# Kernel optimization log

Measured on AMD Instinct MI355X. Metric: run time of the kernel, lower is better.

The kernel has to match this reference:

```python
import jax, jax.numpy as jnp
import numpy as np

EPS = 1e-07
NUM_ELEMENTS = 33554432  # cooptimizer.rest_mesh_blob.num_elements
GRID = (256, 256, 256)   # voxel design grid


def setup_inputs() -> dict:
    key = jax.random.key(0)
    k1, k2 = jax.random.split(key)
    voxel = jax.random.uniform(k1, GRID, dtype=jnp.float32)
    # voxel -> element id map (the keys of blob_to_fish_cell / cell_indices)
    cell_indices = jax.random.randint(k2, GRID, 0, NUM_ELEMENTS, dtype=jnp.int64 if jax.config.jax_enable_x64 else jnp.int32)
    return {"voxel": voxel, "cell_indices": cell_indices, "num_elements": NUM_ELEMENTS}


def reference(voxel, cell_indices, num_elements):
    # clamp matches voxel.clamp(0, 1) (output is value-independent, but kept for fidelity)
    _ = jnp.clip(voxel, 0.0, 1.0)
    # vectorized replacement of `for k in keys: elements[k] = 1.0`
    elements = jnp.zeros((num_elements,), dtype=voxel.dtype).at[cell_indices.reshape(-1)].set(1.0)
    return elements + EPS
```

## Files before the change

kernel.cpp:

```cpp
#include <hip/hip_runtime.h>
#include <hip/hip_bf16.h>

#define EPS   1e-07f
#define ONEPS (1.0f + 1e-07f)

typedef int          iv4 __attribute__((ext_vector_type(4)));
typedef float        fv4 __attribute__((ext_vector_type(4)));
typedef unsigned int uv4 __attribute__((ext_vector_type(4)));

#define NB        512
#define REG       65536
#define SEGCAP    128
#define SEGSTRIDE 136

#define PA_BLOCK 1024
#define PA_CHUNK 32768
#define PA_NBLK  512

#define PB_BLOCK 1024

#define COUNTS_BYTES ((size_t)NB * PA_NBLK)
#define WS_NEEDED    (COUNTS_BYTES + (size_t)NB * PA_NBLK * SEGCAP * 2)

__global__ __launch_bounds__(PA_BLOCK) void bin_kernel(
    const int* __restrict__ idx,
    unsigned short* __restrict__ buckets,
    unsigned char* __restrict__ counts)
{
    __shared__ __align__(16) unsigned short stage[NB * SEGSTRIDE];
    __shared__ int cursor[NB];

    const int t   = threadIdx.x;
    const int blk = blockIdx.x;

    if (t < NB) cursor[t] = 0;
    __syncthreads();

    const iv4* idx4 = (const iv4*)(idx + (size_t)blk * PA_CHUNK);
#pragma unroll 8
    for (int r = 0; r < PA_CHUNK / (PA_BLOCK * 4); ++r) {
        iv4 q = __builtin_nontemporal_load(&idx4[r * PA_BLOCK + t]);
#pragma unroll
        for (int j = 0; j < 4; ++j) {
            int vj = q[j];
            int b = vj >> 16;
            int p = atomicAdd(&cursor[b], 1);
            if (p < SEGCAP)
                stage[b * SEGSTRIDE + p] = (unsigned short)(vj & 0xFFFF);
        }
    }
    __syncthreads();

    if (t < NB) {
        int n_t = cursor[t];
        if (n_t > SEGCAP) n_t = SEGCAP;
        counts[(size_t)blk * NB + t] = (unsigned char)n_t;
    }

    const int w   = t >> 6;
    const int sub = (t >> 4) & 3;
    const int l16 = t & 15;
    for (int i = 0; i < NB / 64; ++i) {
        int b = i * 64 + w * 4 + sub;
        int n = cursor[b];
        if (n > SEGCAP) n = SEGCAP;
        int nu4 = (n + 7) >> 3;
        uv4* dst = (uv4*)(buckets + ((size_t)b * PA_NBLK + blk) * SEGCAP);
        const uv4* srcp = (const uv4*)(stage + b * SEGSTRIDE);
        if (l16 < nu4) {
            uv4 u = srcp[l16];
            if (l16 == nu4 - 1 && (n & 7)) {
                unsigned int e0  = stage[b * SEGSTRIDE];
                unsigned int e00 = e0 | (e0 << 16);
                int base = l16 * 8;
#pragma unroll
                for (int k = 0; k < 4; ++k) {
                    unsigned int wv = u[k];
                    int i0 = base + 2 * k;
                    if (i0 + 1 >= n) wv = (wv & 0xFFFFu) | (e0 << 16);
                    if (i0     >= n) wv = e00;
                    u[k] = wv;
                }
            }
            dst[l16] = u;
        }
    }
}

__global__ __launch_bounds__(PB_BLOCK) void expand_kernel(
    const unsigned short* __restrict__ buckets,
    const unsigned char* __restrict__ counts,
    float* __restrict__ out)
{
    __shared__ unsigned char bm[REG];
    __shared__ unsigned char cnt[PA_NBLK];

    const int t = threadIdx.x;
    const int b = blockIdx.x;

    uint4* bm128 = (uint4*)bm;
#pragma unroll
    for (int i = t; i < REG / 16; i += PB_BLOCK)
        bm128[i] = make_uint4(0u, 0u, 0u, 0u);
    if (t < PA_NBLK)
        cnt[t] = counts[(size_t)t * NB + b];
    __syncthreads();

    const uv4* src4 = (const uv4*)(buckets + (size_t)b * PA_NBLK * SEGCAP);
    const int g   = t >> 4;
    const int l16 = t & 15;
#pragma unroll
    for (int r = 0; r < PA_NBLK / 64; ++r) {
        int seg = r * 64 + g;
        int nu4 = ((int)cnt[seg] + 7) >> 3;
        if (l16 < nu4) {
            uv4 u = src4[seg * (SEGCAP / 8) + l16];
#pragma unroll
            for (int k = 0; k < 4; ++k) {
                unsigned int wv = u[k];
                bm[wv & 0xFFFFu] = 1;
                bm[wv >> 16]     = 1;
            }
        }
    }
    __syncthreads();

    fv4* o = (fv4*)(out + (size_t)b * REG);
    const unsigned int* bm32 = (const unsigned int*)bm;
#pragma unroll 4
    for (int i = t; i < REG / 4; i += PB_BLOCK) {
        unsigned int wv = bm32[i];
        fv4 f;
        f.x = (wv & 0x000000FFu) ? ONEPS : EPS;
        f.y = (wv & 0x0000FF00u) ? ONEPS : EPS;
        f.z = (wv & 0x00FF0000u) ? ONEPS : EPS;
        f.w = (wv & 0xFF000000u) ? ONEPS : EPS;
        __builtin_nontemporal_store(f, &o[i]);
    }
}

__global__ void fill_eps_kernel(float4* __restrict__ out, int n4) {
    int stride = gridDim.x * blockDim.x;
    const float4 v = make_float4(EPS, EPS, EPS, EPS);
    for (int i = blockIdx.x * blockDim.x + threadIdx.x; i < n4; i += stride)
        out[i] = v;
}

__global__ void scatter_ones_kernel(const int4* __restrict__ idx,
                                    float* __restrict__ out, int n4) {
    int i = blockIdx.x * blockDim.x + threadIdx.x;
    if (i < n4) {
        int4 v = idx[i];
        out[v.x] = ONEPS;
        out[v.y] = ONEPS;
        out[v.z] = ONEPS;
        out[v.w] = ONEPS;
    }
}

extern "C" void kernel_launch(void* const* d_in, const int* in_sizes, int n_in,
                              void* d_out, int out_size, void* d_ws, size_t ws_size,
                              hipStream_t stream) {
    const int* cell_indices = (const int*)d_in[1];
    const int n_idx = in_sizes[1];

    if (out_size == NB * REG && n_idx == PA_NBLK * PA_CHUNK &&
        ws_size >= WS_NEEDED) {
        unsigned char* counts = (unsigned char*)d_ws;
        unsigned short* buckets =
            (unsigned short*)((char*)d_ws + COUNTS_BYTES);

        bin_kernel<<<PA_NBLK, PA_BLOCK, 0, stream>>>(
            cell_indices, buckets, counts);

        expand_kernel<<<NB, PB_BLOCK, 0, stream>>>(
            buckets, counts, (float*)d_out);
    } else {
        int n4_fill = out_size >> 2;
        fill_eps_kernel<<<2048, 256, 0, stream>>>((float4*)d_out, n4_fill);
        int n4_idx = n_idx >> 2;
        int blocks = (n4_idx + 255) / 256;
        scatter_ones_kernel<<<blocks, 256, 0, stream>>>(
            (const int4*)cell_indices, (float*)d_out, n4_idx);
    }
}
```

Before: 61.74 us.

## Use bit-packed LDS bitmap with atomicOr and transpose counts layout in expand

The expand kernel's 64 KB byte-per-element LDS bitmap becomes an 8 KB bit-packed bitmap updated with LDS atomicOr, and the block size drops to 512 threads. The smaller LDS footprint lets several blocks share a CU instead of one, and zeroing the bitmap is cheaper. The counts array is now written transposed by the binning kernel so each expand block reads its counts contiguously with 32-bit loads. The cost is atomic read-modify-write in place of plain byte stores, which can serialize when lanes hit the same word, plus extra shift work when converting bits to floats.

```diff
diff --git a/kernel.cpp b/kernel.cpp
--- a/kernel.cpp
+++ b/kernel.cpp
@@ -17,7 +17,7 @@
 #define PA_CHUNK 32768
 #define PA_NBLK  512
 
-#define PB_BLOCK 1024
+#define PB_BLOCK 512
 
 #define COUNTS_BYTES ((size_t)NB * PA_NBLK)
 #define WS_NEEDED    (COUNTS_BYTES + (size_t)NB * PA_NBLK * SEGCAP * 2)
@@ -54,7 +54,7 @@
     if (t < NB) {
         int n_t = cursor[t];
         if (n_t > SEGCAP) n_t = SEGCAP;
-        counts[(size_t)blk * NB + t] = (unsigned char)n_t;
+        counts[(size_t)t * PA_NBLK + blk] = (unsigned char)n_t;
     }
 
     const int w   = t >> 6;
@@ -92,49 +92,49 @@
     const unsigned char* __restrict__ counts,
     float* __restrict__ out)
 {
-    __shared__ unsigned char bm[REG];
+    __shared__ unsigned int bm[REG / 32];
     __shared__ unsigned char cnt[PA_NBLK];
 
     const int t = threadIdx.x;
     const int b = blockIdx.x;
 
-    uint4* bm128 = (uint4*)bm;
-#pragma unroll
-    for (int i = t; i < REG / 16; i += PB_BLOCK)
-        bm128[i] = make_uint4(0u, 0u, 0u, 0u);
-    if (t < PA_NBLK)
-        cnt[t] = counts[(size_t)t * NB + b];
+    ((uint4*)bm)[t] = make_uint4(0u, 0u, 0u, 0u);
+    if (t < PA_NBLK / 4)
+        ((unsigned int*)cnt)[t] =
+            ((const unsigned int*)(counts + (size_t)b * PA_NBLK))[t];
     __syncthreads();
 
     const uv4* src4 = (const uv4*)(buckets + (size_t)b * PA_NBLK * SEGCAP);
     const int g   = t >> 4;
     const int l16 = t & 15;
 #pragma unroll
-    for (int r = 0; r < PA_NBLK / 64; ++r) {
-        int seg = r * 64 + g;
+    for (int r = 0; r < PA_NBLK / 32; ++r) {
+        int seg = r * 32 + g;
         int nu4 = ((int)cnt[seg] + 7) >> 3;
         if (l16 < nu4) {
             uv4 u = src4[seg * (SEGCAP / 8) + l16];
 #pragma unroll
             for (int k = 0; k < 4; ++k) {
                 unsigned int wv = u[k];
-                bm[wv & 0xFFFFu] = 1;
-                bm[wv >> 16]     = 1;
+                unsigned int e0 = wv & 0xFFFFu;
+                unsigned int e1 = wv >> 16;
+                atomicOr(&bm[e0 >> 5], 1u << (e0 & 31));
+                atomicOr(&bm[e1 >> 5], 1u << (e1 & 31));
             }
         }
     }
     __syncthreads();
 
     fv4* o = (fv4*)(out + (size_t)b * REG);
-    const unsigned int* bm32 = (const unsigned int*)bm;
 #pragma unroll 4
     for (int i = t; i < REG / 4; i += PB_BLOCK) {
-        unsigned int wv = bm32[i];
+        unsigned int wv = bm[i >> 3];
+        int s = (i & 7) * 4;
         fv4 f;
-        f.x = (wv & 0x000000FFu) ? ONEPS : EPS;
-        f.y = (wv & 0x0000FF00u) ? ONEPS : EPS;
-        f.z = (wv & 0x00FF0000u) ? ONEPS : EPS;
-        f.w = (wv & 0xFF000000u) ? ONEPS : EPS;
+        f.x = ((wv >> (s + 0)) & 1u) ? ONEPS : EPS;
+        f.y = ((wv >> (s + 1)) & 1u) ? ONEPS : EPS;
+        f.z = ((wv >> (s + 2)) & 1u) ? ONEPS : EPS;
+        f.w = ((wv >> (s + 3)) & 1u) ? ONEPS : EPS;
         __builtin_nontemporal_store(f, &o[i]);
     }
 }
```

After: 63.70 us. 1.03x slower.
